# Optimization experiments

Measured on AMD Instinct MI355X. Metric: run time of the kernel, lower is better.

Reference implementation:

```python
import jax, jax.numpy as jnp
import numpy as np

ATOM_FDIM = 35
BOND_FDIM = 5
MAX_NB = 10
HIDDEN = 128
DEPTH = 6
A = 131072   # total atoms
B = 262144   # total directed bonds
M = 32768    # tree messages (row 0 is the zero pad vector, as in the torch code)
N_MOLS = 4096


def setup_inputs() -> dict:
    key = jax.random.key(0)
    ks = jax.random.split(key, 9)
    atom_feats = jax.random.uniform(ks[0], (A, ATOM_FDIM), dtype=jnp.float32)
    bond_feats = jax.random.uniform(ks[1], (B, ATOM_FDIM + BOND_FDIM), dtype=jnp.float32)
    tree_message = jax.random.normal(ks[2], (M, HIDDEN), dtype=jnp.float32)
    tree_message = tree_message.at[0].set(0.0)  # all_mess[0] = zeros padding
    atom_graph = jax.random.randint(ks[3], (A, MAX_NB), 0, M + B)
    bond_graph = jax.random.randint(ks[4], (B, MAX_NB), 0, M + B)
    s = 1.0 / np.sqrt(HIDDEN)
    W_i = jax.random.uniform(ks[5], (HIDDEN, ATOM_FDIM + BOND_FDIM), jnp.float32, -s, s)
    W_h = jax.random.uniform(ks[6], (HIDDEN, HIDDEN), jnp.float32, -s, s)
    W_o = jax.random.uniform(ks[7], (HIDDEN, ATOM_FDIM + HIDDEN), jnp.float32, -s, s)
    b_o = jax.random.uniform(ks[8], (HIDDEN,), jnp.float32, -s, s)
    return {"atom_feats": atom_feats, "bond_feats": bond_feats,
            "tree_message": tree_message, "atom_graph": atom_graph,
            "bond_graph": bond_graph, "n_mols": N_MOLS,
            "W_i": W_i, "W_h": W_h, "W_o": W_o, "b_o": b_o}


def reference(atom_feats, bond_feats, tree_message, atom_graph, bond_graph,
              n_mols, W_i, W_h, W_o, b_o):
    # h0 = ReLU(W_i @ bond_feats): [B, H]
    h0 = jax.nn.relu(jnp.einsum('bf,hf->bh', bond_feats, W_i))
    graph_message = h0
    for _ in range(DEPTH - 1):
        message = jnp.concatenate([tree_message, graph_message], axis=0)  # [M+B, H]
        nei = jnp.take(message, bond_graph, axis=0).sum(axis=1)           # [B, H]
        graph_message = jax.nn.relu(h0 + jnp.einsum('bh,gh->bg', nei, W_h))
    message = jnp.concatenate([tree_message, graph_message], axis=0)
    nei_a = jnp.take(message, atom_graph, axis=0).sum(axis=1)             # [A, H]
    atom_in = jnp.concatenate([atom_feats, nei_a], axis=1)                # [A, F+H]
    atom_hiddens = jax.nn.relu(jnp.einsum('af,hf->ah', atom_in, W_o) + b_o)
    # per-molecule mean over equal-size contiguous scopes
    atoms_per_mol = A // n_mols
    mol_ids = jnp.arange(A) // atoms_per_mol
    mol_vecs = jax.ops.segment_sum(atom_hiddens, mol_ids, num_segments=n_mols)
    return mol_vecs / atoms_per_mol
```

## Files before the change

### kernel.cpp

```cpp
#include <hip/hip_runtime.h>

#define H       128
#define MAXNB   10
#define M_TREE  32768
#define NBOND   262144
#define NATOM   131072
#define FATOM   35
#define FBOND   40
#define FOUT    163
#define KPAD    192
#define NMOLS   4096
#define APM     32
#define TB      128

typedef __bf16 bf16x8 __attribute__((ext_vector_type(8)));
typedef float  f32x4  __attribute__((ext_vector_type(4)));

__device__ __forceinline__ unsigned short f32_to_bf16(float f) {
  unsigned int u = __float_as_uint(f);
  u += 0x7FFFu + ((u >> 16) & 1u);
  return (unsigned short)(u >> 16);
}
__device__ __forceinline__ float bf16u_to_f32(unsigned short h) {
  return __uint_as_float(((unsigned int)h) << 16);
}

__global__ __launch_bounds__(256) void prep(const float* __restrict__ tm,
                                            const float* __restrict__ wh,
                                            const float* __restrict__ wo,
                                            const float* __restrict__ wi,
                                            unsigned short* __restrict__ tmsg,
                                            unsigned short* __restrict__ whb,
                                            unsigned short* __restrict__ wob,
                                            unsigned short* __restrict__ wib) {
  int i = blockIdx.x * 256 + threadIdx.x;
  const int n1 = M_TREE * H;
  const int n2 = H * H;
  const int n3 = H * KPAD;
  const int n4 = H * 64;
  if (i < n1) { tmsg[i] = f32_to_bf16(tm[i]); return; }
  int j = i - n1;
  if (j < n2) { whb[j] = f32_to_bf16(wh[j]); return; }
  int k = j - n2;
  if (k < n3) {
    int g = k / KPAD, kk = k - g * KPAD;
    float v = 0.f;
    if (kk < 35)                 v = wo[g * FOUT + kk];
    else if (kk >= 36 && kk < 164) v = wo[g * FOUT + kk - 1];
    wob[k] = f32_to_bf16(v);
    return;
  }
  int m = k - n3;
  if (m < n4) {
    int g = m / 64, kk = m - g * 64;
    wib[m] = (kk < FBOND) ? f32_to_bf16(wi[g * FBOND + kk]) : (unsigned short)0;
  }
}

__global__ __launch_bounds__(256, 3) void wi_gemm(const float* __restrict__ bond_feats,
                                                  const unsigned short* __restrict__ wib,
                                                  unsigned short* __restrict__ h0) {
  __shared__ unsigned short sF[128][72];
  const int t = threadIdx.x;
  const int lane = t & 63;
  const int wave = t >> 6;
  const int n16 = lane & 15;
  const int quad = lane >> 4;
  const int b0 = blockIdx.x * 128;

  for (int i = t; i < 128 * FBOND; i += 256) {
    int b = i / FBOND, f = i - b * FBOND;
    sF[b][f] = f32_to_bf16(bond_feats[b0 * FBOND + i]);
  }
  for (int i = t; i < 128 * 24; i += 256) {
    int b = i / 24, c = 40 + i - b * 24;
    sF[b][c] = 0;
  }
  bf16x8 Bf[2][2];
#pragma unroll
  for (int kt = 0; kt < 2; ++kt)
#pragma unroll
    for (int nt = 0; nt < 2; ++nt)
      Bf[kt][nt] = *(const bf16x8*)(wib + ((wave * 2 + nt) * 16 + n16) * 64 + kt * 32 + quad * 8);
  __syncthreads();

  f32x4 acc[8][2];
  f32x4 zero = {0.f, 0.f, 0.f, 0.f};
#pragma unroll
  for (int mt = 0; mt < 8; ++mt) { acc[mt][0] = zero; acc[mt][1] = zero; }
#pragma unroll
  for (int kt = 0; kt < 2; ++kt)
#pragma unroll
    for (int mt = 0; mt < 8; ++mt) {
      bf16x8 av = *(const bf16x8*)&sF[mt * 16 + n16][kt * 32 + quad * 8];
      acc[mt][0] = __builtin_amdgcn_mfma_f32_16x16x32_bf16(av, Bf[kt][0], acc[mt][0], 0, 0, 0);
      acc[mt][1] = __builtin_amdgcn_mfma_f32_16x16x32_bf16(av, Bf[kt][1], acc[mt][1], 0, 0, 0);
    }
#pragma unroll
  for (int mt = 0; mt < 8; ++mt)
#pragma unroll
    for (int nt = 0; nt < 2; ++nt) {
      const int col = (wave * 2 + nt) * 16 + n16;
#pragma unroll
      for (int r = 0; r < 4; ++r) {
        const int b = b0 + mt * 16 + quad * 4 + r;
        h0[b * H + col] = f32_to_bf16(fmaxf(acc[mt][nt][r], 0.f));
      }
    }
}

__global__ __launch_bounds__(256, 3) void mp_step(const unsigned short* __restrict__ gm_in,
                                                  unsigned short* __restrict__ gm_out,
                                                  const unsigned short* __restrict__ h0,
                                                  const unsigned short* __restrict__ tmsg,
                                                  const int* __restrict__ bond_graph,
                                                  const unsigned short* __restrict__ whb) {
  __shared__ unsigned short snei[TB][136];
  __shared__ int sBG[TB * MAXNB];
  const int t = threadIdx.x;
  const int lane = t & 63;
  const int wave = t >> 6;
  const int n16 = lane & 15;
  const int quad = lane >> 4;
  const int b0 = blockIdx.x * TB;

  for (int i = t; i < TB * MAXNB; i += 256) sBG[i] = bond_graph[b0 * MAXNB + i];

  bf16x8 Bf[4][2];
#pragma unroll
  for (int kt = 0; kt < 4; ++kt)
#pragma unroll
    for (int nt = 0; nt < 2; ++nt)
      Bf[kt][nt] = *(const bf16x8*)(whb + ((wave * 2 + nt) * 16 + n16) * H + kt * 32 + quad * 8);
  __syncthreads();

  const unsigned short* gsh = gm_in - (size_t)M_TREE * H;
  for (int lb = wave * 2; lb < TB; lb += 8) {
    unsigned int u[2][MAXNB];
#pragma unroll
    for (int p = 0; p < 2; ++p) {
      const int* ig = &sBG[(lb + p) * MAXNB];
#pragma unroll
      for (int j = 0; j < MAXNB; ++j) {
        int idx = ig[j];
        const unsigned short* r = ((idx < M_TREE) ? tmsg : gsh) + (size_t)idx * H;
        u[p][j] = *(const unsigned int*)(r + 2 * lane);
      }
    }
#pragma unroll
    for (int p = 0; p < 2; ++p) {
      float a0 = 0.f, a1 = 0.f;
#pragma unroll
      for (int j = 0; j < MAXNB; ++j) {
        a0 += __uint_as_float(u[p][j] << 16);
        a1 += __uint_as_float(u[p][j] & 0xFFFF0000u);
      }
      unsigned int packed = ((unsigned int)f32_to_bf16(a1) << 16) | (unsigned int)f32_to_bf16(a0);
      *(unsigned int*)&snei[lb + p][2 * lane] = packed;
    }
  }
  __syncthreads();

  f32x4 acc[8][2];
  f32x4 zero = {0.f, 0.f, 0.f, 0.f};
#pragma unroll
  for (int mt = 0; mt < 8; ++mt) { acc[mt][0] = zero; acc[mt][1] = zero; }
#pragma unroll
  for (int kt = 0; kt < 4; ++kt)
#pragma unroll
    for (int mt = 0; mt < 8; ++mt) {
      bf16x8 av = *(const bf16x8*)&snei[mt * 16 + n16][kt * 32 + quad * 8];
      acc[mt][0] = __builtin_amdgcn_mfma_f32_16x16x32_bf16(av, Bf[kt][0], acc[mt][0], 0, 0, 0);
      acc[mt][1] = __builtin_amdgcn_mfma_f32_16x16x32_bf16(av, Bf[kt][1], acc[mt][1], 0, 0, 0);
    }

#pragma unroll
  for (int mt = 0; mt < 8; ++mt)
#pragma unroll
    for (int nt = 0; nt < 2; ++nt) {
      const int col = (wave * 2 + nt) * 16 + n16;
#pragma unroll
      for (int r = 0; r < 4; ++r) {
        const int b = b0 + mt * 16 + quad * 4 + r;
        float hv = bf16u_to_f32(h0[b * H + col]);
        gm_out[b * H + col] = f32_to_bf16(fmaxf(hv + acc[mt][nt][r], 0.f));
      }
    }
}

__global__ __launch_bounds__(256, 3) void readout(const float* __restrict__ atom_feats,
                                                  const unsigned short* __restrict__ gm,
                                                  const unsigned short* __restrict__ tmsg,
                                                  const int* __restrict__ atom_graph,
                                                  const unsigned short* __restrict__ wob,
                                                  const float* __restrict__ b_o,
                                                  float* __restrict__ out) {
  __shared__ unsigned short sA[128][200];
  __shared__ int sAG[128 * MAXNB];
  const int t = threadIdx.x;
  const int lane = t & 63;
  const int wave = t >> 6;
  const int n16 = lane & 15;
  const int quad = lane >> 4;
  const int blk = blockIdx.x;
  const int abase = blk * 128;

  for (int i = t; i < 128 * MAXNB; i += 256) sAG[i] = atom_graph[abase * MAXNB + i];
  for (int i = t; i < 128 * FATOM; i += 256) {
    int a = i / FATOM, f = i - a * FATOM;
    sA[a][f] = f32_to_bf16(atom_feats[abase * FATOM + i]);
  }
  if (t < 128) sA[t][35] = 0;
  for (int i = t; i < 128 * 28; i += 256) {
    int a = i / 28, c = 164 + i - a * 28;
    sA[a][c] = 0;
  }

  bf16x8 Bf[6][2];
#pragma unroll
  for (int kt = 0; kt < 6; ++kt)
#pragma unroll
    for (int nt = 0; nt < 2; ++nt)
      Bf[kt][nt] = *(const bf16x8*)(wob + ((wave * 2 + nt) * 16 + n16) * KPAD + kt * 32 + quad * 8);
  __syncthreads();

  const unsigned short* gsh = gm - (size_t)M_TREE * H;
  for (int la = wave * 2; la < 128; la += 8) {
    unsigned int u[2][MAXNB];
#pragma unroll
    for (int p = 0; p < 2; ++p) {
      const int* ig = &sAG[(la + p) * MAXNB];
#pragma unroll
      for (int j = 0; j < MAXNB; ++j) {
        int idx = ig[j];
        const unsigned short* r = ((idx < M_TREE) ? tmsg : gsh) + (size_t)idx * H;
        u[p][j] = *(const unsigned int*)(r + 2 * lane);
      }
    }
#pragma unroll
    for (int p = 0; p < 2; ++p) {
      float a0 = 0.f, a1 = 0.f;
#pragma unroll
      for (int j = 0; j < MAXNB; ++j) {
        a0 += __uint_as_float(u[p][j] << 16);
        a1 += __uint_as_float(u[p][j] & 0xFFFF0000u);
      }
      unsigned int packed = ((unsigned int)f32_to_bf16(a1) << 16) | (unsigned int)f32_to_bf16(a0);
      *(unsigned int*)&sA[la + p][36 + 2 * lane] = packed;
    }
  }
  __syncthreads();

  f32x4 acc[8][2];
  f32x4 zero = {0.f, 0.f, 0.f, 0.f};
#pragma unroll
  for (int mt = 0; mt < 8; ++mt) { acc[mt][0] = zero; acc[mt][1] = zero; }
#pragma unroll
  for (int kt = 0; kt < 6; ++kt)
#pragma unroll
    for (int mt = 0; mt < 8; ++mt) {
      bf16x8 av = *(const bf16x8*)&sA[mt * 16 + n16][kt * 32 + quad * 8];
      acc[mt][0] = __builtin_amdgcn_mfma_f32_16x16x32_bf16(av, Bf[kt][0], acc[mt][0], 0, 0, 0);
      acc[mt][1] = __builtin_amdgcn_mfma_f32_16x16x32_bf16(av, Bf[kt][1], acc[mt][1], 0, 0, 0);
    }

  float bo[2] = { b_o[(wave * 2) * 16 + n16], b_o[(wave * 2 + 1) * 16 + n16] };
  float part[4][2] = {{0.f,0.f},{0.f,0.f},{0.f,0.f},{0.f,0.f}};
#pragma unroll
  for (int mt = 0; mt < 8; ++mt)
#pragma unroll
    for (int nt = 0; nt < 2; ++nt)
#pragma unroll
      for (int r = 0; r < 4; ++r)
        part[mt >> 1][nt] += fmaxf(acc[mt][nt][r] + bo[nt], 0.f);
#pragma unroll
  for (int mol = 0; mol < 4; ++mol)
#pragma unroll
    for (int nt = 0; nt < 2; ++nt) {
      float p = part[mol][nt];
      p += __shfl_xor(p, 16);
      p += __shfl_xor(p, 32);
      if (lane < 16)
        out[(blk * 4 + mol) * H + (wave * 2 + nt) * 16 + lane] = p * (1.0f / APM);
    }
}

extern "C" void kernel_launch(void* const* d_in, const int* in_sizes, int n_in,
                              void* d_out, int out_size, void* d_ws, size_t ws_size,
                              hipStream_t stream) {
  (void)in_sizes; (void)n_in; (void)out_size; (void)ws_size;
  const float* atom_feats   = (const float*)d_in[0];
  const float* bond_feats   = (const float*)d_in[1];
  const float* tree_message = (const float*)d_in[2];
  const int*   atom_graph   = (const int*)d_in[3];
  const int*   bond_graph   = (const int*)d_in[4];
  const float* W_i = (const float*)d_in[6];
  const float* W_h = (const float*)d_in[7];
  const float* W_o = (const float*)d_in[8];
  const float* b_o = (const float*)d_in[9];
  float* out = (float*)d_out;

  char* ws = (char*)d_ws;
  unsigned short* tmsg = (unsigned short*)(ws);
  unsigned short* whb  = (unsigned short*)(ws + 8388608);
  unsigned short* wob  = (unsigned short*)(ws + 8421376);
  unsigned short* wib  = (unsigned short*)(ws + 8470528);
  unsigned short* h0   = (unsigned short*)(ws + 8486912);
  unsigned short* gm0  = (unsigned short*)(ws + 75595776);
  unsigned short* gm1  = (unsigned short*)(ws + 142704640);

  prep<<<16576, 256, 0, stream>>>(tree_message, W_h, W_o, W_i, tmsg, whb, wob, wib);
  wi_gemm<<<NBOND / 128, 256, 0, stream>>>(bond_feats, wib, h0);
  mp_step<<<NBOND / TB, 256, 0, stream>>>(h0,  gm0, h0, tmsg, bond_graph, whb);
  mp_step<<<NBOND / TB, 256, 0, stream>>>(gm0, gm1, h0, tmsg, bond_graph, whb);
  mp_step<<<NBOND / TB, 256, 0, stream>>>(gm1, gm0, h0, tmsg, bond_graph, whb);
  mp_step<<<NBOND / TB, 256, 0, stream>>>(gm0, gm1, h0, tmsg, bond_graph, whb);
  mp_step<<<NBOND / TB, 256, 0, stream>>>(gm1, gm0, h0, tmsg, bond_graph, whb);
  readout<<<NATOM / 128, 256, 0, stream>>>(atom_feats, gm0, tmsg, atom_graph, wob, b_o, out);
}
```

Before: 866.4 us.

## Stage mp_step epilogue through LDS for coalesced stores and scalarize gather indices

```diff
diff --git a/kernel.cpp b/kernel.cpp
--- a/kernel.cpp
+++ b/kernel.cpp
@@ -15,6 +15,7 @@
 
 typedef __bf16 bf16x8 __attribute__((ext_vector_type(8)));
 typedef float  f32x4  __attribute__((ext_vector_type(4)));
+typedef unsigned int u32x4 __attribute__((ext_vector_type(4)));
 
 __device__ __forceinline__ unsigned short f32_to_bf16(float f) {
   unsigned int u = __float_as_uint(f);
@@ -23,6 +24,12 @@
 }
 __device__ __forceinline__ float bf16u_to_f32(unsigned short h) {
   return __uint_as_float(((unsigned int)h) << 16);
+}
+__device__ __forceinline__ unsigned int bfpair_addrelu(unsigned int a, unsigned int h) {
+  float a0 = __uint_as_float(a << 16), a1 = __uint_as_float(a & 0xFFFF0000u);
+  float h0v = __uint_as_float(h << 16), h1v = __uint_as_float(h & 0xFFFF0000u);
+  float r0 = fmaxf(a0 + h0v, 0.f), r1 = fmaxf(a1 + h1v, 0.f);
+  return ((unsigned int)f32_to_bf16(r1) << 16) | (unsigned int)f32_to_bf16(r0);
 }
 
 __global__ __launch_bounds__(256) void prep(const float* __restrict__ tm,
@@ -38,14 +45,14 @@
   const int n2 = H * H;
   const int n3 = H * KPAD;
   const int n4 = H * 64;
-  if (i < n1) { tmsg[i] = f32_to_bf16(tm[i]); return; }
+  if (i < n1) { tmsg[i] = f32_to_bf16(__builtin_nontemporal_load(tm + i)); return; }
   int j = i - n1;
   if (j < n2) { whb[j] = f32_to_bf16(wh[j]); return; }
   int k = j - n2;
   if (k < n3) {
     int g = k / KPAD, kk = k - g * KPAD;
     float v = 0.f;
-    if (kk < 35)                 v = wo[g * FOUT + kk];
+    if (kk < 35)                   v = wo[g * FOUT + kk];
     else if (kk >= 36 && kk < 164) v = wo[g * FOUT + kk - 1];
     wob[k] = f32_to_bf16(v);
     return;
@@ -70,7 +77,7 @@
 
   for (int i = t; i < 128 * FBOND; i += 256) {
     int b = i / FBOND, f = i - b * FBOND;
-    sF[b][f] = f32_to_bf16(bond_feats[b0 * FBOND + i]);
+    sF[b][f] = f32_to_bf16(__builtin_nontemporal_load(bond_feats + b0 * FBOND + i));
   }
   for (int i = t; i < 128 * 24; i += 256) {
     int b = i / 24, c = 40 + i - b * 24;
@@ -109,7 +116,7 @@
     }
 }
 
-__global__ __launch_bounds__(256, 3) void mp_step(const unsigned short* __restrict__ gm_in,
+__global__ __launch_bounds__(256, 4) void mp_step(const unsigned short* __restrict__ gm_in,
                                                   unsigned short* __restrict__ gm_out,
                                                   const unsigned short* __restrict__ h0,
                                                   const unsigned short* __restrict__ tmsg,
@@ -124,14 +131,8 @@
   const int quad = lane >> 4;
   const int b0 = blockIdx.x * TB;
 
-  for (int i = t; i < TB * MAXNB; i += 256) sBG[i] = bond_graph[b0 * MAXNB + i];
-
-  bf16x8 Bf[4][2];
-#pragma unroll
-  for (int kt = 0; kt < 4; ++kt)
-#pragma unroll
-    for (int nt = 0; nt < 2; ++nt)
-      Bf[kt][nt] = *(const bf16x8*)(whb + ((wave * 2 + nt) * 16 + n16) * H + kt * 32 + quad * 8);
+  for (int i = t; i < TB * MAXNB; i += 256)
+    sBG[i] = __builtin_nontemporal_load(bond_graph + b0 * MAXNB + i);
   __syncthreads();
 
   const unsigned short* gsh = gm_in - (size_t)M_TREE * H;
@@ -142,7 +143,7 @@
       const int* ig = &sBG[(lb + p) * MAXNB];
 #pragma unroll
       for (int j = 0; j < MAXNB; ++j) {
-        int idx = ig[j];
+        int idx = __builtin_amdgcn_readfirstlane(ig[j]);
         const unsigned short* r = ((idx < M_TREE) ? tmsg : gsh) + (size_t)idx * H;
         u[p][j] = *(const unsigned int*)(r + 2 * lane);
       }
@@ -159,6 +160,13 @@
       *(unsigned int*)&snei[lb + p][2 * lane] = packed;
     }
   }
+
+  bf16x8 Bf[4][2];
+#pragma unroll
+  for (int kt = 0; kt < 4; ++kt)
+#pragma unroll
+    for (int nt = 0; nt < 2; ++nt)
+      Bf[kt][nt] = *(const bf16x8*)(whb + ((wave * 2 + nt) * 16 + n16) * H + kt * 32 + quad * 8);
   __syncthreads();
 
   f32x4 acc[8][2];
@@ -173,6 +181,7 @@
       acc[mt][0] = __builtin_amdgcn_mfma_f32_16x16x32_bf16(av, Bf[kt][0], acc[mt][0], 0, 0, 0);
       acc[mt][1] = __builtin_amdgcn_mfma_f32_16x16x32_bf16(av, Bf[kt][1], acc[mt][1], 0, 0, 0);
     }
+  __syncthreads();
 
 #pragma unroll
   for (int mt = 0; mt < 8; ++mt)
@@ -180,12 +189,26 @@
     for (int nt = 0; nt < 2; ++nt) {
       const int col = (wave * 2 + nt) * 16 + n16;
 #pragma unroll
-      for (int r = 0; r < 4; ++r) {
-        const int b = b0 + mt * 16 + quad * 4 + r;
-        float hv = bf16u_to_f32(h0[b * H + col]);
-        gm_out[b * H + col] = f32_to_bf16(fmaxf(hv + acc[mt][nt][r], 0.f));
-      }
-    }
+      for (int r = 0; r < 4; ++r)
+        snei[mt * 16 + quad * 4 + r][col] = f32_to_bf16(acc[mt][nt][r]);
+    }
+  __syncthreads();
+
+  const size_t gbase = (size_t)b0 * H;
+#pragma unroll
+  for (int c = 0; c < 8; ++c) {
+    int fl = c * 256 + t;
+    int row = fl >> 4;
+    int col = (fl & 15) * 8;
+    u32x4 a4 = *(const u32x4*)&snei[row][col];
+    u32x4 h4 = __builtin_nontemporal_load((const u32x4*)(h0 + gbase + (size_t)row * H + col));
+    u32x4 o4;
+    o4.x = bfpair_addrelu(a4.x, h4.x);
+    o4.y = bfpair_addrelu(a4.y, h4.y);
+    o4.z = bfpair_addrelu(a4.z, h4.z);
+    o4.w = bfpair_addrelu(a4.w, h4.w);
+    *(u32x4*)(gm_out + gbase + (size_t)row * H + col) = o4;
+  }
 }
 
 __global__ __launch_bounds__(256, 3) void readout(const float* __restrict__ atom_feats,
@@ -205,23 +228,17 @@
   const int blk = blockIdx.x;
   const int abase = blk * 128;
 
-  for (int i = t; i < 128 * MAXNB; i += 256) sAG[i] = atom_graph[abase * MAXNB + i];
+  for (int i = t; i < 128 * MAXNB; i += 256)
+    sAG[i] = __builtin_nontemporal_load(atom_graph + abase * MAXNB + i);
   for (int i = t; i < 128 * FATOM; i += 256) {
     int a = i / FATOM, f = i - a * FATOM;
-    sA[a][f] = f32_to_bf16(atom_feats[abase * FATOM + i]);
+    sA[a][f] = f32_to_bf16(__builtin_nontemporal_load(atom_feats + abase * FATOM + i));
   }
   if (t < 128) sA[t][35] = 0;
   for (int i = t; i < 128 * 28; i += 256) {
     int a = i / 28, c = 164 + i - a * 28;
     sA[a][c] = 0;
   }
-
-  bf16x8 Bf[6][2];
-#pragma unroll
-  for (int kt = 0; kt < 6; ++kt)
-#pragma unroll
-    for (int nt = 0; nt < 2; ++nt)
-      Bf[kt][nt] = *(const bf16x8*)(wob + ((wave * 2 + nt) * 16 + n16) * KPAD + kt * 32 + quad * 8);
   __syncthreads();
 
   const unsigned short* gsh = gm - (size_t)M_TREE * H;
@@ -232,7 +249,7 @@
       const int* ig = &sAG[(la + p) * MAXNB];
 #pragma unroll
       for (int j = 0; j < MAXNB; ++j) {
-        int idx = ig[j];
+        int idx = __builtin_amdgcn_readfirstlane(ig[j]);
         const unsigned short* r = ((idx < M_TREE) ? tmsg : gsh) + (size_t)idx * H;
         u[p][j] = *(const unsigned int*)(r + 2 * lane);
       }
@@ -249,6 +266,13 @@
       *(unsigned int*)&sA[la + p][36 + 2 * lane] = packed;
     }
   }
+
+  bf16x8 Bf[6][2];
+#pragma unroll
+  for (int kt = 0; kt < 6; ++kt)
+#pragma unroll
+    for (int nt = 0; nt < 2; ++nt)
+      Bf[kt][nt] = *(const bf16x8*)(wob + ((wave * 2 + nt) * 16 + n16) * KPAD + kt * 32 + quad * 8);
   __syncthreads();
 
   f32x4 acc[8][2];
```

Result: faster. 812.4 us (-6.2%).
